# Kernel optimization log

Measured on AMD Instinct MI355X. Metric: run time of the kernel, lower is better.

The kernel has to match this reference:

```python
import jax, jax.numpy as jnp
import numpy as np

EPS = 1e-6
LOG2PI = float(np.log(2.0 * np.pi))


def gauss_lp(x, mu, lv):
    """Diagonal Gaussian log prob. x:[B,D], mu:[K,D], lv:[K,D] -> [B,K]."""
    inv_var = jnp.exp(-lv)                          # [K,D]
    d = x[:, None, :] - mu[None, :, :]              # [B,K,D]
    quad = jnp.sum(d * d * inv_var[None], axis=-1)  # [B,K]
    logdet = jnp.sum(lv, axis=-1)[None]             # [1,K]
    D = mu.shape[-1]
    return -0.5 * (quad + logdet + D * LOG2PI)


def setup_inputs() -> dict:
    key = jax.random.key(0)
    ks = jax.random.split(key, 9)
    T, B, S, A, OBS, CTL = 200, 256, 256, 16, 128, 16
    return {
        "x": jax.random.normal(ks[0], (T, B, OBS), jnp.float32),
        "u": jax.random.normal(ks[1], (T, B, CTL), jnp.float32),
        "obs_mu": jax.random.normal(ks[2], (S, OBS), jnp.float32),
        "obs_lv": 0.1 * jax.random.normal(ks[3], (S, OBS), jnp.float32),
        "ctl_mu": jax.random.normal(ks[4], (A, CTL), jnp.float32),
        "ctl_lv": 0.1 * jax.random.normal(ks[5], (A, CTL), jnp.float32),
        "trans_logits": jax.random.normal(ks[6], (A, S, S), jnp.float32),
        "pi0_logits": jax.random.normal(ks[7], (S,), jnp.float32),
        "act_prior": jax.random.normal(ks[8], (S, A), jnp.float32),
    }


def reference(x, u, obs_mu, obs_lv, ctl_mu, ctl_lv, trans_logits, pi0_logits, act_prior):
    """HMM forward algorithm (ContinuousGaussianHMM._forward).

    Returns:
      alpha_b: [T, B, S] state forward messages
      alpha_a: [T-1, B, A] action forward messages
    """
    S = obs_mu.shape[0]
    trans = jax.nn.softmax(trans_logits, axis=-1)      # [A,S,S]
    log_pi0 = jax.nn.log_softmax(pi0_logits)           # [S]

    # t = 0: initial state prior + observation likelihood
    b0 = jax.nn.softmax(gauss_lp(x[0], obs_mu, obs_lv) + log_pi0[None], axis=-1)  # [B,S]

    def step(b, xu):
        x_t, u_t = xu
        # action prior from belief: softmax(b @ act_prior)
        a_prior = jax.nn.softmax(b @ act_prior, axis=-1)                           # [B,A]
        # ctl_model.infer: posterior over actions given control u_t
        a_t = jax.nn.softmax(gauss_lp(u_t, ctl_mu, ctl_lv) + jnp.log(a_prior + EPS), axis=-1)  # [B,A]
        # action-conditioned transition applied to belief
        m = jnp.einsum('bi,kij->bkj', b, trans)                                    # [B,A,S]
        # original: sum_i(trans*b + eps) => einsum + S*eps
        logp_z = jnp.log(jnp.einsum('bk,bkj->bj', a_t, m) + S * EPS)               # [B,S]
        b_next = jax.nn.softmax(gauss_lp(x_t, obs_mu, obs_lv) + logp_z, axis=-1)   # [B,S]
        return b_next, (b_next, a_t)

    _, (bs, a_s) = jax.lax.scan(step, b0, (x[1:], u[:-1]))
    alpha_b = jnp.concatenate([b0[None], bs], axis=0)   # [T,B,S]
    alpha_a = a_s                                       # [T-1,B,A]
    return alpha_b, alpha_a
```

## Files before the change

kernel.cpp:

```cpp
#include <hip/hip_runtime.h>
#include <hip/hip_bf16.h>
#include <stdint.h>

#define T_STEPS 200
#define BATCH   256
#define NS      256
#define NA      16
#define DOBS    128
#define DCTL    16
#define LOG2PI  1.8378770664093453f
#define EPS_F   1e-6f
#define MINI(a,b) ((a)<(b)?(a):(b))

typedef float f32x4 __attribute__((ext_vector_type(4)));
typedef int   i32x4 __attribute__((ext_vector_type(4)));
typedef short s16x8 __attribute__((ext_vector_type(8)));
typedef short s16x4 __attribute__((ext_vector_type(4)));

static __device__ __forceinline__ unsigned short f2bf(float f) {
    union { float f; unsigned u; } v; v.f = f;
    unsigned u = v.u;
    u += 0x7fffu + ((u >> 16) & 1u);
    return (unsigned short)(u >> 16);
}

static __device__ __forceinline__ void ld4_mall(const float* base,
                                                f32x4& a, f32x4& b, f32x4& c, f32x4& d) {
    asm volatile(
        "global_load_dwordx4 %0, %4, off offset:0 sc0 sc1\n\t"
        "global_load_dwordx4 %1, %4, off offset:1024 sc0 sc1\n\t"
        "global_load_dwordx4 %2, %4, off offset:2048 sc0 sc1\n\t"
        "global_load_dwordx4 %3, %4, off offset:3072 sc0 sc1\n\t"
        "s_waitcnt vmcnt(0)"
        : "=&v"(a), "=&v"(b), "=&v"(c), "=&v"(d)
        : "v"(base)
        : "memory");
}
static __device__ __forceinline__ void st_mall(float* p, f32x4 v) {
    asm volatile("global_store_dwordx4 %0, %1, off sc0 sc1" :: "v"(p), "v"(v) : "memory");
}
static __device__ __forceinline__ void st_flag(int* p, int v) {
    asm volatile("global_store_dword %0, %1, off sc0 sc1" :: "v"(p), "v"(v) : "memory");
}
static __device__ __forceinline__ int min16(const int* fp) {
    i32x4 a, b, c, d;
    asm volatile(
        "global_load_dwordx4 %0, %4, off offset:0 sc0 sc1\n\t"
        "global_load_dwordx4 %1, %4, off offset:16 sc0 sc1\n\t"
        "global_load_dwordx4 %2, %4, off offset:32 sc0 sc1\n\t"
        "global_load_dwordx4 %3, %4, off offset:48 sc0 sc1\n\t"
        "s_waitcnt vmcnt(0)"
        : "=&v"(a), "=&v"(b), "=&v"(c), "=&v"(d)
        : "v"(fp)
        : "memory");
    int m = MINI(MINI(a[0], a[1]), MINI(a[2], a[3]));
    m = MINI(m, MINI(MINI(b[0], b[1]), MINI(b[2], b[3])));
    m = MINI(m, MINI(MINI(c[0], c[1]), MINI(c[2], c[3])));
    m = MINI(m, MINI(MINI(d[0], d[1]), MINI(d[2], d[3])));
    return m;
}

__global__ __launch_bounds__(128) void k_prep_obs(const float* __restrict__ obs_mu,
                                                  const float* __restrict__ obs_lv,
                                                  float* __restrict__ WT,
                                                  float* __restrict__ Cs) {
    int s = blockIdx.x, d = threadIdx.x;
    float lv = obs_lv[s * DOBS + d];
    float mu = obs_mu[s * DOBS + d];
    float iv = expf(-lv);
    WT[d * NS + s]          = -0.5f * iv;
    WT[(DOBS + d) * NS + s] = mu * iv;
    float part = mu * mu * iv + lv;
    for (int m = 1; m < 64; m <<= 1) part += __shfl_xor(part, m, 64);
    __shared__ float red[2];
    if ((threadIdx.x & 63) == 0) red[threadIdx.x >> 6] = part;
    __syncthreads();
    if (threadIdx.x == 0) Cs[s] = -0.5f * (red[0] + red[1] + DOBS * LOG2PI);
}

__global__ __launch_bounds__(256) void k_prep_ctl(const float* __restrict__ cmu,
                                                  const float* __restrict__ clv,
                                                  float* __restrict__ cw1,
                                                  float* __restrict__ cw2,
                                                  float* __restrict__ cc) {
    int t = threadIdx.x;
    int a = t >> 4, d = t & 15;
    float lv = clv[a * DCTL + d];
    float mu = cmu[a * DCTL + d];
    float iv = expf(-lv);
    cw1[t] = -0.5f * iv;
    cw2[t] = mu * iv;
    float part = mu * mu * iv + lv;
    for (int m = 1; m < 16; m <<= 1) part += __shfl_xor(part, m, 64);
    if (d == 0) cc[a] = -0.5f * (part + DCTL * LOG2PI);
}

__global__ __launch_bounds__(64) void k_prep_pi0(const float* __restrict__ pl,
                                                 float* __restrict__ lpi0) {
    int l = threadIdx.x;
    float v[4]; float m = -1e30f;
    for (int k = 0; k < 4; k++) { v[k] = pl[l + 64 * k]; m = fmaxf(m, v[k]); }
    for (int mm = 1; mm < 64; mm <<= 1) m = fmaxf(m, __shfl_xor(m, mm, 64));
    float ssum = 0.f;
    for (int k = 0; k < 4; k++) ssum += expf(v[k] - m);
    for (int mm = 1; mm < 64; mm <<= 1) ssum += __shfl_xor(ssum, mm, 64);
    float ls = logf(ssum);
    for (int k = 0; k < 4; k++) lpi0[l + 64 * k] = v[k] - m - ls;
}

__global__ __launch_bounds__(256) void k_zero(int* __restrict__ f) {
    st_flag(f + threadIdx.x, 0);
}

__global__ __launch_bounds__(256) void k_trans(const float* __restrict__ tl,
                                               __hip_bfloat16* __restrict__ TRf) {
    int wave = threadIdx.x >> 6, lane = threadIdx.x & 63;
    int row = blockIdx.x * 4 + wave;
    int a = row >> 8, i = row & 255;
    const float* src = tl + (size_t)row * NS;
    float v[4]; float m = -1e30f;
    for (int k = 0; k < 4; k++) { v[k] = src[lane + 64 * k]; m = fmaxf(m, v[k]); }
    for (int mm = 1; mm < 64; mm <<= 1) m = fmaxf(m, __shfl_xor(m, mm, 64));
    float ssum = 0.f; float ev[4];
    for (int k = 0; k < 4; k++) { ev[k] = expf(v[k] - m); ssum += ev[k]; }
    for (int mm = 1; mm < 64; mm <<= 1) ssum += __shfl_xor(ssum, mm, 64);
    float inv = 1.f / ssum;
    int kk = i >> 5;
    int lsub = ((i >> 3) & 3) * 16 + a;
    int e = i & 7;
    for (int k = 0; k < 4; k++) {
        int j = lane + 64 * k;
        float p = ev[k] * inv;
        TRf[((size_t)(j * 8 + kk) * 64 + lsub) * 8 + e] = __float2bfloat16(p);
    }
}

__global__ __launch_bounds__(64) void k_prep_ap(const float* __restrict__ ap,
                                                __hip_bfloat16* __restrict__ APh,
                                                __hip_bfloat16* __restrict__ APl) {
    int kk = blockIdx.x, lane = threadIdx.x;
    for (int e = 0; e < 8; e++) {
        int i = kk * 32 + (lane >> 4) * 8 + e;
        int a = lane & 15;
        float v = ap[i * NA + a];
        __hip_bfloat16 hb = __float2bfloat16(v);
        float hi = __bfloat162float(hb);
        APh[(kk * 64 + lane) * 8 + e] = hb;
        APl[(kk * 64 + lane) * 8 + e] = __float2bfloat16(v - hi);
    }
}

__global__ __launch_bounds__(256) void k_obslp(const float* __restrict__ x,
                                               const float* __restrict__ WT,
                                               const float* __restrict__ Cs,
                                               float* __restrict__ obs) {
    __shared__ float f[32 * 256];
    int r0 = blockIdx.x * 32;
    for (int idx = threadIdx.x; idx < 32 * DOBS; idx += 256) {
        int r = idx >> 7, d = idx & 127;
        float v = x[(size_t)(r0 + r) * DOBS + d];
        f[r * 256 + d] = v * v;
        f[r * 256 + 128 + d] = v;
    }
    __syncthreads();
    int s = threadIdx.x;
    float acc[32];
#pragma unroll
    for (int r = 0; r < 32; r++) acc[r] = 0.f;
    for (int d4 = 0; d4 < 64; d4++) {
        float w0 = WT[(d4 * 4 + 0) * NS + s];
        float w1 = WT[(d4 * 4 + 1) * NS + s];
        float w2 = WT[(d4 * 4 + 2) * NS + s];
        float w3 = WT[(d4 * 4 + 3) * NS + s];
#pragma unroll
        for (int r = 0; r < 32; r++) {
            f32x4 fv = *reinterpret_cast<const f32x4*>(&f[r * 256 + d4 * 4]);
            acc[r] += fv.x * w0 + fv.y * w1 + fv.z * w2 + fv.w * w3;
        }
    }
    float c = Cs[s];
#pragma unroll
    for (int r = 0; r < 32; r++) obs[(size_t)(r0 + r) * NS + s] = acc[r] + c;
}

__global__ __launch_bounds__(256) void k_ctllp(const float* __restrict__ u,
                                               const float* __restrict__ cw1,
                                               const float* __restrict__ cw2,
                                               const float* __restrict__ cc,
                                               float* __restrict__ ctl) {
    int idx = blockIdx.x * 256 + threadIdx.x;
    int r = idx >> 4, a = idx & 15;
    const float* ur = u + (size_t)r * DCTL;
    const float* w1 = cw1 + a * DCTL;
    const float* w2 = cw2 + a * DCTL;
    float acc = cc[a];
#pragma unroll
    for (int d = 0; d < 16; d++) {
        float uv = ur[d];
        acc += uv * uv * w1[d] + uv * w2[d];
    }
    ctl[idx] = acc;
}

struct ScanArgs {
    const float* obs;
    const float* ctlp;
    const float* lpi0;
    const __hip_bfloat16* TRf;
    const __hip_bfloat16* APh;
    const __hip_bfloat16* APl;
    float* lgA;
    float* lgB;
    float* out_ab;
    float* out_aa;
    int*   flags;
};

__global__ __launch_bounds__(256, 1) void k_scan_p(ScanArgs A) {
    const int bid  = blockIdx.x;
    const int bt   = bid >> 4;
    const int jt   = bid & 15;
    const int tid  = threadIdx.x;
    const int wv   = tid >> 6, lane = tid & 63;
    const int kgrp = lane >> 4, arow = lane & 15;
    const int b0   = bt * 16;
    const int* fp  = A.flags + bt * 16;

    __shared__ __align__(16) char PLb[16 * 512];
    __shared__ float out_t[16][16];

    s16x8 bfr[4][8];
#pragma unroll
    for (int q = 0; q < 4; q++) {
        int ct = jt * 16 + wv * 4 + q;
#pragma unroll
        for (int kk = 0; kk < 8; kk++)
            bfr[q][kk] = *((const s16x8*)A.TRf + (size_t)(ct * 8 + kk) * 64 + lane);
    }
    s16x8 aph[8], apl[8];
#pragma unroll
    for (int kk = 0; kk < 8; kk++) {
        aph[kk] = *((const s16x8*)A.APh + kk * 64 + lane);
        apl[kk] = *((const s16x8*)A.APl + kk * 64 + lane);
    }
    f32x4 lp0 = *(const f32x4*)&A.lpi0[lane * 4];

    const float* obs_pf_p = A.obs + ((size_t)BATCH + b0 + kgrp * 4) * NS + jt * 16 + wv * 4;
    const float* ctl_p    = A.ctlp + ((size_t)b0 + kgrp * 4) * NA + arow;
    float*       ab_p     = A.out_ab + ((size_t)b0 + wv * 4) * NS + lane * 4;
    float*       aa_p     = A.out_aa + ((size_t)b0 + kgrp * 4) * NA + arow;
    const float* lgA_ld   = A.lgA + ((size_t)b0 + wv * 4) * NS + lane * 4;
    const float* lgB_ld   = A.lgB + ((size_t)b0 + wv * 4) * NS + lane * 4;
    float*       lgA_st   = A.lgA + ((size_t)b0 + (lane >> 2)) * NS + jt * 16 + (lane & 3) * 4;
    float*       lgB_st   = A.lgB + ((size_t)b0 + (lane >> 2)) * NS + jt * 16 + (lane & 3) * 4;

    for (int s = 0; s < T_STEPS - 1; s++) {
        float obs_pf[16];
#pragma unroll
        for (int q2 = 0; q2 < 4; q2++)
#pragma unroll
            for (int r = 0; r < 4; r++)
                obs_pf[q2 * 4 + r] = obs_pf_p[r * NS + q2];
        float ctl_pf[4];
#pragma unroll
        for (int q = 0; q < 4; q++)
            ctl_pf[q] = ctl_p[q * NA];

        if (s > 0) {
            if (tid == 0) {
                while (min16(fp) < s) __builtin_amdgcn_s_sleep(1);
            }
            __syncthreads();
        }

        f32x4 V[4];
        if (s == 0) {
#pragma unroll
            for (int q = 0; q < 4; q++) {
                f32x4 o = *(const f32x4*)&A.obs[(size_t)(b0 + wv * 4 + q) * NS + lane * 4];
                V[q] = o + lp0;
            }
        } else {
            ld4_mall((s & 1) ? lgB_ld : lgA_ld, V[0], V[1], V[2], V[3]);
        }
#pragma unroll
        for (int q = 0; q < 4; q++) {
            int r = wv * 4 + q;
            float m = fmaxf(fmaxf(V[q].x, V[q].y), fmaxf(V[q].z, V[q].w));
            for (int mm = 1; mm < 64; mm <<= 1) m = fmaxf(m, __shfl_xor(m, mm, 64));
            float e0 = __expf(V[q].x - m), e1 = __expf(V[q].y - m);
            float e2 = __expf(V[q].z - m), e3 = __expf(V[q].w - m);
            float ss = (e0 + e1) + (e2 + e3);
            for (int mm = 1; mm < 64; mm <<= 1) ss += __shfl_xor(ss, mm, 64);
            float inv = 1.f / ss;
            float p0 = e0 * inv, p1 = e1 * inv, p2 = e2 * inv, p3 = e3 * inv;
            if ((lane >> 2) == jt) {
                f32x4 pv = {p0, p1, p2, p3};
                *(f32x4*)&ab_p[q * NS] = pv;
            }
            s16x4 sv;
            sv[0] = (short)f2bf(p0); sv[1] = (short)f2bf(p1);
            sv[2] = (short)f2bf(p2); sv[3] = (short)f2bf(p3);
            *(s16x4*)(PLb + r * 512 + ((lane * 8) ^ ((r & 7) << 4))) = sv;
        }
        __syncthreads();

        s16x8 afr[8];
        {
            int sw = (arow & 7) << 4;
#pragma unroll
            for (int kk = 0; kk < 8; kk++)
                afr[kk] = *(const s16x8*)(PLb + arow * 512 + ((kk * 64 + kgrp * 16) ^ sw));
        }

        f32x4 g = {0.f, 0.f, 0.f, 0.f};
#pragma unroll
        for (int kk = 0; kk < 8; kk++)
            g = __builtin_amdgcn_mfma_f32_16x16x32_bf16(afr[kk], aph[kk], g, 0, 0, 0);
#pragma unroll
        for (int kk = 0; kk < 8; kk++)
            g = __builtin_amdgcn_mfma_f32_16x16x32_bf16(afr[kk], apl[kk], g, 0, 0, 0);

        float at[4];
#pragma unroll
        for (int q = 0; q < 4; q++) {
            float gv = g[q];
            float m = gv;
            for (int mm = 1; mm < 16; mm <<= 1) m = fmaxf(m, __shfl_xor(m, mm, 64));
            float e1 = __expf(gv - m);
            float s1 = e1;
            for (int mm = 1; mm < 16; mm <<= 1) s1 += __shfl_xor(s1, mm, 64);
            float apr = e1 / s1;
            float al = ctl_pf[q] + __logf(apr + EPS_F);
            float m2 = al;
            for (int mm = 1; mm < 16; mm <<= 1) m2 = fmaxf(m2, __shfl_xor(m2, mm, 64));
            float e2 = __expf(al - m2);
            float s2 = e2;
            for (int mm = 1; mm < 16; mm <<= 1) s2 += __shfl_xor(s2, mm, 64);
            at[q] = e2 / s2;
            if (jt == 0)
                aa_p[q * NA] = at[q];
        }

#pragma unroll
        for (int q2 = 0; q2 < 4; q2++) {
            f32x4 acc = {0.f, 0.f, 0.f, 0.f};
#pragma unroll
            for (int kk = 0; kk < 8; kk++)
                acc = __builtin_amdgcn_mfma_f32_16x16x32_bf16(afr[kk], bfr[q2][kk], acc, 0, 0, 0);
#pragma unroll
            for (int r = 0; r < 4; r++) {
                float vv = acc[r] * at[r];
                for (int mm = 1; mm < 16; mm <<= 1) vv += __shfl_xor(vv, mm, 64);
                if (arow == 0)
                    out_t[kgrp * 4 + r][wv * 4 + q2] =
                        obs_pf[q2 * 4 + r] + __logf(vv + NS * EPS_F);
            }
        }
        __syncthreads();

        if (wv == 0) {
            f32x4 val = *(const f32x4*)&out_t[lane >> 2][(lane & 3) * 4];
            st_mall((s & 1) ? lgA_st : lgB_st, val);
            asm volatile("s_waitcnt vmcnt(0)" ::: "memory");
            if (lane == 0)
                st_flag((int*)&A.flags[bt * 16 + jt], s + 1);
        }
        obs_pf_p += (size_t)BATCH * NS;
        ctl_p    += (size_t)BATCH * NA;
        ab_p     += (size_t)BATCH * NS;
        aa_p     += (size_t)BATCH * NA;
    }

    if (tid == 0) {
        while (min16(fp) < T_STEPS - 1) __builtin_amdgcn_s_sleep(1);
    }
    __syncthreads();
    f32x4 V[4];
    ld4_mall(((T_STEPS - 1) & 1) ? lgB_ld : lgA_ld, V[0], V[1], V[2], V[3]);
#pragma unroll
    for (int q = 0; q < 4; q++) {
        float m = fmaxf(fmaxf(V[q].x, V[q].y), fmaxf(V[q].z, V[q].w));
        for (int mm = 1; mm < 64; mm <<= 1) m = fmaxf(m, __shfl_xor(m, mm, 64));
        float e0 = __expf(V[q].x - m), e1 = __expf(V[q].y - m);
        float e2 = __expf(V[q].z - m), e3 = __expf(V[q].w - m);
        float ss = (e0 + e1) + (e2 + e3);
        for (int mm = 1; mm < 64; mm <<= 1) ss += __shfl_xor(ss, mm, 64);
        float inv = 1.f / ss;
        if ((lane >> 2) == jt) {
            f32x4 pv = {e0 * inv, e1 * inv, e2 * inv, e3 * inv};
            *(f32x4*)&ab_p[q * NS] = pv;
        }
    }
}

extern "C" void kernel_launch(void* const* d_in, const int* in_sizes, int n_in,
                              void* d_out, int out_size, void* d_ws, size_t ws_size,
                              hipStream_t stream) {
    const float* x            = (const float*)d_in[0];
    const float* u            = (const float*)d_in[1];
    const float* obs_mu       = (const float*)d_in[2];
    const float* obs_lv       = (const float*)d_in[3];
    const float* ctl_mu       = (const float*)d_in[4];
    const float* ctl_lv       = (const float*)d_in[5];
    const float* trans_logits = (const float*)d_in[6];
    const float* pi0_logits   = (const float*)d_in[7];
    const float* act_prior    = (const float*)d_in[8];

    float* out_ab = (float*)d_out;
    float* out_aa = out_ab + (size_t)T_STEPS * BATCH * NS;

    char* w = (char*)d_ws;
    size_t off = 0;
    auto alloc = [&](size_t bytes) -> void* {
        void* pp = w + off;
        off += (bytes + 255) & ~(size_t)255;
        return pp;
    };
    float* WT   = (float*)alloc((size_t)256 * 256 * 4);
    float* Cs   = (float*)alloc(256 * 4);
    float* cw1  = (float*)alloc(256 * 4);
    float* cw2  = (float*)alloc(256 * 4);
    float* cc   = (float*)alloc(16 * 4);
    float* lpi0 = (float*)alloc(256 * 4);
    __hip_bfloat16* TRf = (__hip_bfloat16*)alloc((size_t)4096 * 256 * 2);
    __hip_bfloat16* APh = (__hip_bfloat16*)alloc((size_t)8 * 64 * 8 * 2);
    __hip_bfloat16* APl = (__hip_bfloat16*)alloc((size_t)8 * 64 * 8 * 2);
    float* obs  = (float*)alloc((size_t)T_STEPS * BATCH * NS * 4);
    float* ctlp = (float*)alloc((size_t)(T_STEPS - 1) * BATCH * NA * 4);
    float* lgA  = (float*)alloc((size_t)BATCH * NS * 4);
    float* lgB  = (float*)alloc((size_t)BATCH * NS * 4);
    int*   flags = (int*)alloc(256 * 4);
    if (off > ws_size) return;

    k_zero<<<1, 256, 0, stream>>>(flags);
    k_prep_obs<<<256, 128, 0, stream>>>(obs_mu, obs_lv, WT, Cs);
    k_prep_ctl<<<1, 256, 0, stream>>>(ctl_mu, ctl_lv, cw1, cw2, cc);
    k_prep_pi0<<<1, 64, 0, stream>>>(pi0_logits, lpi0);
    k_trans<<<1024, 256, 0, stream>>>(trans_logits, TRf);
    k_prep_ap<<<8, 64, 0, stream>>>(act_prior, APh, APl);
    k_obslp<<<1600, 256, 0, stream>>>(x, WT, Cs, obs);
    k_ctllp<<<3184, 256, 0, stream>>>(u, cw1, cw2, cc, ctlp);

    ScanArgs args;
    args.obs = obs; args.ctlp = ctlp; args.lpi0 = lpi0;
    args.TRf = TRf; args.APh = APh; args.APl = APl;
    args.lgA = lgA; args.lgB = lgB;
    args.out_ab = out_ab; args.out_aa = out_aa; args.flags = flags;
    k_scan_p<<<256, 256, 0, stream>>>(args);
}
```

Before: 2.366 ms.

## Split each scan block into two interleaved 8-row batch groups with blocked exchange layout

Each persistent scan block now handles two independent groups of 8 batch rows, 32 groups in total, and alternates their steps. While one group waits on its cross-block flags, the other can compute, which is meant to hide synchronisation latency between blocks. The lgA/lgB exchange buffers move to a per-tile blocked layout so each block stores one contiguous 512-byte chunk. MFMA tiles are half padded with zero rows, which wastes compute and adds extra barriers per step.

```diff
diff --git a/kernel.cpp b/kernel.cpp
--- a/kernel.cpp
+++ b/kernel.cpp
@@ -24,17 +24,12 @@
     return (unsigned short)(u >> 16);
 }
 
-static __device__ __forceinline__ void ld4_mall(const float* base,
-                                                f32x4& a, f32x4& b, f32x4& c, f32x4& d) {
+static __device__ __forceinline__ void ld2_mall(const float* base, f32x4& a, f32x4& b) {
     asm volatile(
-        "global_load_dwordx4 %0, %4, off offset:0 sc0 sc1\n\t"
-        "global_load_dwordx4 %1, %4, off offset:1024 sc0 sc1\n\t"
-        "global_load_dwordx4 %2, %4, off offset:2048 sc0 sc1\n\t"
-        "global_load_dwordx4 %3, %4, off offset:3072 sc0 sc1\n\t"
+        "global_load_dwordx4 %0, %2, off offset:0 sc0 sc1\n\t"
+        "global_load_dwordx4 %1, %2, off offset:64 sc0 sc1\n\t"
         "s_waitcnt vmcnt(0)"
-        : "=&v"(a), "=&v"(b), "=&v"(c), "=&v"(d)
-        : "v"(base)
-        : "memory");
+        : "=&v"(a), "=&v"(b) : "v"(base) : "memory");
 }
 static __device__ __forceinline__ void st_mall(float* p, f32x4 v) {
     asm volatile("global_store_dwordx4 %0, %1, off sc0 sc1" :: "v"(p), "v"(v) : "memory");
@@ -108,7 +103,7 @@
     for (int k = 0; k < 4; k++) lpi0[l + 64 * k] = v[k] - m - ls;
 }
 
-__global__ __launch_bounds__(256) void k_zero(int* __restrict__ f) {
+__global__ __launch_bounds__(512) void k_zero(int* __restrict__ f) {
     st_flag(f + threadIdx.x, 0);
 }
 
@@ -216,170 +211,133 @@
     int*   flags;
 };
 
-__global__ __launch_bounds__(256, 1) void k_scan_p(ScanArgs A) {
-    const int bid  = blockIdx.x;
-    const int bt   = bid >> 4;
-    const int jt   = bid & 15;
-    const int tid  = threadIdx.x;
-    const int wv   = tid >> 6, lane = tid & 63;
-    const int kgrp = lane >> 4, arow = lane & 15;
-    const int b0   = bt * 16;
-    const int* fp  = A.flags + bt * 16;
-
-    __shared__ __align__(16) char PLb[16 * 512];
-    __shared__ float out_t[16][16];
-
-    s16x8 bfr[4][8];
-#pragma unroll
-    for (int q = 0; q < 4; q++) {
-        int ct = jt * 16 + wv * 4 + q;
-#pragma unroll
-        for (int kk = 0; kk < 8; kk++)
-            bfr[q][kk] = *((const s16x8*)A.TRf + (size_t)(ct * 8 + kk) * 64 + lane);
-    }
-    s16x8 aph[8], apl[8];
-#pragma unroll
-    for (int kk = 0; kk < 8; kk++) {
-        aph[kk] = *((const s16x8*)A.APh + kk * 64 + lane);
-        apl[kk] = *((const s16x8*)A.APl + kk * 64 + lane);
-    }
-    f32x4 lp0 = *(const f32x4*)&A.lpi0[lane * 4];
-
-    const float* obs_pf_p = A.obs + ((size_t)BATCH + b0 + kgrp * 4) * NS + jt * 16 + wv * 4;
-    const float* ctl_p    = A.ctlp + ((size_t)b0 + kgrp * 4) * NA + arow;
-    float*       ab_p     = A.out_ab + ((size_t)b0 + wv * 4) * NS + lane * 4;
-    float*       aa_p     = A.out_aa + ((size_t)b0 + kgrp * 4) * NA + arow;
-    const float* lgA_ld   = A.lgA + ((size_t)b0 + wv * 4) * NS + lane * 4;
-    const float* lgB_ld   = A.lgB + ((size_t)b0 + wv * 4) * NS + lane * 4;
-    float*       lgA_st   = A.lgA + ((size_t)b0 + (lane >> 2)) * NS + jt * 16 + (lane & 3) * 4;
-    float*       lgB_st   = A.lgB + ((size_t)b0 + (lane >> 2)) * NS + jt * 16 + (lane & 3) * 4;
-
-    for (int s = 0; s < T_STEPS - 1; s++) {
-        float obs_pf[16];
-#pragma unroll
-        for (int q2 = 0; q2 < 4; q2++)
-#pragma unroll
-            for (int r = 0; r < 4; r++)
-                obs_pf[q2 * 4 + r] = obs_pf_p[r * NS + q2];
-        float ctl_pf[4];
-#pragma unroll
-        for (int q = 0; q < 4; q++)
-            ctl_pf[q] = ctl_p[q * NA];
-
-        if (s > 0) {
-            if (tid == 0) {
-                while (min16(fp) < s) __builtin_amdgcn_s_sleep(1);
-            }
-            __syncthreads();
-        }
-
-        f32x4 V[4];
-        if (s == 0) {
-#pragma unroll
-            for (int q = 0; q < 4; q++) {
-                f32x4 o = *(const f32x4*)&A.obs[(size_t)(b0 + wv * 4 + q) * NS + lane * 4];
-                V[q] = o + lp0;
-            }
-        } else {
-            ld4_mall((s & 1) ? lgB_ld : lgA_ld, V[0], V[1], V[2], V[3]);
-        }
-#pragma unroll
-        for (int q = 0; q < 4; q++) {
-            int r = wv * 4 + q;
-            float m = fmaxf(fmaxf(V[q].x, V[q].y), fmaxf(V[q].z, V[q].w));
-            for (int mm = 1; mm < 64; mm <<= 1) m = fmaxf(m, __shfl_xor(m, mm, 64));
-            float e0 = __expf(V[q].x - m), e1 = __expf(V[q].y - m);
-            float e2 = __expf(V[q].z - m), e3 = __expf(V[q].w - m);
-            float ss = (e0 + e1) + (e2 + e3);
-            for (int mm = 1; mm < 64; mm <<= 1) ss += __shfl_xor(ss, mm, 64);
-            float inv = 1.f / ss;
-            float p0 = e0 * inv, p1 = e1 * inv, p2 = e2 * inv, p3 = e3 * inv;
-            if ((lane >> 2) == jt) {
-                f32x4 pv = {p0, p1, p2, p3};
-                *(f32x4*)&ab_p[q * NS] = pv;
-            }
-            s16x4 sv;
-            sv[0] = (short)f2bf(p0); sv[1] = (short)f2bf(p1);
-            sv[2] = (short)f2bf(p2); sv[3] = (short)f2bf(p3);
-            *(s16x4*)(PLb + r * 512 + ((lane * 8) ^ ((r & 7) << 4))) = sv;
+static __device__ __forceinline__ void scan_step(
+    int s, int jt, int lane, int wv, int kgrp, int arow,
+    const s16x8 (&bfr)[4][8], const s16x8 (&aph)[8], const s16x8 (&apl)[8],
+    const f32x4& lp0,
+    const float*& obs_pf_p, const float*& ctl_p, float*& ab_p, float*& aa_p,
+    const float* obs0, const float* lgA_ld, const float* lgB_ld,
+    float* lgA_st, float* lgB_st,
+    const int* flagline, int* ownslot,
+    char* PLb, float (*out_t)[16])
+{
+    f32x4 obs_pfv[4];
+#pragma unroll
+    for (int r = 0; r < 4; r++)
+        obs_pfv[r] = *(const f32x4*)&obs_pf_p[r * NS];
+    float ctl_pf[4];
+#pragma unroll
+    for (int q = 0; q < 4; q++)
+        ctl_pf[q] = ctl_p[q * NA];
+
+    if (s > 0) {
+        if (threadIdx.x == 0) {
+            while (min16(flagline) < s) __builtin_amdgcn_s_sleep(1);
         }
         __syncthreads();
-
-        s16x8 afr[8];
-        {
-            int sw = (arow & 7) << 4;
-#pragma unroll
-            for (int kk = 0; kk < 8; kk++)
-                afr[kk] = *(const s16x8*)(PLb + arow * 512 + ((kk * 64 + kgrp * 16) ^ sw));
+    }
+
+    f32x4 V[2];
+    if (s == 0) {
+        V[0] = *(const f32x4*)&obs0[0]  + lp0;
+        V[1] = *(const f32x4*)&obs0[NS] + lp0;
+    } else {
+        ld2_mall((s & 1) ? lgB_ld : lgA_ld, V[0], V[1]);
+    }
+#pragma unroll
+    for (int q = 0; q < 2; q++) {
+        int r = wv * 2 + q;
+        float m = fmaxf(fmaxf(V[q].x, V[q].y), fmaxf(V[q].z, V[q].w));
+        for (int mm = 1; mm < 64; mm <<= 1) m = fmaxf(m, __shfl_xor(m, mm, 64));
+        float e0 = __expf(V[q].x - m), e1 = __expf(V[q].y - m);
+        float e2 = __expf(V[q].z - m), e3 = __expf(V[q].w - m);
+        float ss = (e0 + e1) + (e2 + e3);
+        for (int mm = 1; mm < 64; mm <<= 1) ss += __shfl_xor(ss, mm, 64);
+        float inv = 1.f / ss;
+        float p0 = e0 * inv, p1 = e1 * inv, p2 = e2 * inv, p3 = e3 * inv;
+        if ((lane >> 2) == jt) {
+            f32x4 pv = {p0, p1, p2, p3};
+            *(f32x4*)&ab_p[q * NS] = pv;
         }
-
-        f32x4 g = {0.f, 0.f, 0.f, 0.f};
+        s16x4 sv;
+        sv[0] = (short)f2bf(p0); sv[1] = (short)f2bf(p1);
+        sv[2] = (short)f2bf(p2); sv[3] = (short)f2bf(p3);
+        *(s16x4*)(PLb + r * 512 + ((lane * 8) ^ (r << 4))) = sv;
+    }
+    __syncthreads();
+
+    s16x8 afr[8];
+    {
+        int sw = (arow & 7) << 4;
 #pragma unroll
         for (int kk = 0; kk < 8; kk++)
-            g = __builtin_amdgcn_mfma_f32_16x16x32_bf16(afr[kk], aph[kk], g, 0, 0, 0);
+            afr[kk] = *(const s16x8*)(PLb + arow * 512 + ((kk * 64 + kgrp * 16) ^ sw));
+    }
+
+    f32x4 gh = {0.f, 0.f, 0.f, 0.f}, gl = {0.f, 0.f, 0.f, 0.f};
+#pragma unroll
+    for (int kk = 0; kk < 8; kk++) {
+        gh = __builtin_amdgcn_mfma_f32_16x16x32_bf16(afr[kk], aph[kk], gh, 0, 0, 0);
+        gl = __builtin_amdgcn_mfma_f32_16x16x32_bf16(afr[kk], apl[kk], gl, 0, 0, 0);
+    }
+    float at[4];
+#pragma unroll
+    for (int q = 0; q < 4; q++) {
+        float gv = gh[q] + gl[q];
+        float m = gv;
+        for (int mm = 1; mm < 16; mm <<= 1) m = fmaxf(m, __shfl_xor(m, mm, 64));
+        float e1 = __expf(gv - m);
+        float s1 = e1;
+        for (int mm = 1; mm < 16; mm <<= 1) s1 += __shfl_xor(s1, mm, 64);
+        float apr = e1 / s1;
+        float al = ctl_pf[q] + __logf(apr + EPS_F);
+        float m2 = al;
+        for (int mm = 1; mm < 16; mm <<= 1) m2 = fmaxf(m2, __shfl_xor(m2, mm, 64));
+        float e2 = __expf(al - m2);
+        float s2 = e2;
+        for (int mm = 1; mm < 16; mm <<= 1) s2 += __shfl_xor(s2, mm, 64);
+        at[q] = e2 / s2;
+        if (jt == 0 && kgrp < 2)
+            aa_p[q * NA] = at[q];
+    }
+
+#pragma unroll
+    for (int q2 = 0; q2 < 4; q2++) {
+        f32x4 acc = {0.f, 0.f, 0.f, 0.f};
 #pragma unroll
         for (int kk = 0; kk < 8; kk++)
-            g = __builtin_amdgcn_mfma_f32_16x16x32_bf16(afr[kk], apl[kk], g, 0, 0, 0);
-
-        float at[4];
-#pragma unroll
-        for (int q = 0; q < 4; q++) {
-            float gv = g[q];
-            float m = gv;
-            for (int mm = 1; mm < 16; mm <<= 1) m = fmaxf(m, __shfl_xor(m, mm, 64));
-            float e1 = __expf(gv - m);
-            float s1 = e1;
-            for (int mm = 1; mm < 16; mm <<= 1) s1 += __shfl_xor(s1, mm, 64);
-            float apr = e1 / s1;
-            float al = ctl_pf[q] + __logf(apr + EPS_F);
-            float m2 = al;
-            for (int mm = 1; mm < 16; mm <<= 1) m2 = fmaxf(m2, __shfl_xor(m2, mm, 64));
-            float e2 = __expf(al - m2);
-            float s2 = e2;
-            for (int mm = 1; mm < 16; mm <<= 1) s2 += __shfl_xor(s2, mm, 64);
-            at[q] = e2 / s2;
-            if (jt == 0)
-                aa_p[q * NA] = at[q];
+            acc = __builtin_amdgcn_mfma_f32_16x16x32_bf16(afr[kk], bfr[q2][kk], acc, 0, 0, 0);
+#pragma unroll
+        for (int r = 0; r < 4; r++) {
+            float vv = acc[r] * at[r];
+            for (int mm = 1; mm < 16; mm <<= 1) vv += __shfl_xor(vv, mm, 64);
+            if (arow == 0 && kgrp < 2)
+                out_t[kgrp * 4 + r][wv * 4 + q2] =
+                    obs_pfv[r][q2] + __logf(vv + NS * EPS_F);
         }
-
-#pragma unroll
-        for (int q2 = 0; q2 < 4; q2++) {
-            f32x4 acc = {0.f, 0.f, 0.f, 0.f};
-#pragma unroll
-            for (int kk = 0; kk < 8; kk++)
-                acc = __builtin_amdgcn_mfma_f32_16x16x32_bf16(afr[kk], bfr[q2][kk], acc, 0, 0, 0);
-#pragma unroll
-            for (int r = 0; r < 4; r++) {
-                float vv = acc[r] * at[r];
-                for (int mm = 1; mm < 16; mm <<= 1) vv += __shfl_xor(vv, mm, 64);
-                if (arow == 0)
-                    out_t[kgrp * 4 + r][wv * 4 + q2] =
-                        obs_pf[q2 * 4 + r] + __logf(vv + NS * EPS_F);
-            }
-        }
-        __syncthreads();
-
-        if (wv == 0) {
-            f32x4 val = *(const f32x4*)&out_t[lane >> 2][(lane & 3) * 4];
-            st_mall((s & 1) ? lgA_st : lgB_st, val);
-            asm volatile("s_waitcnt vmcnt(0)" ::: "memory");
-            if (lane == 0)
-                st_flag((int*)&A.flags[bt * 16 + jt], s + 1);
-        }
-        obs_pf_p += (size_t)BATCH * NS;
-        ctl_p    += (size_t)BATCH * NA;
-        ab_p     += (size_t)BATCH * NS;
-        aa_p     += (size_t)BATCH * NA;
-    }
-
-    if (tid == 0) {
-        while (min16(fp) < T_STEPS - 1) __builtin_amdgcn_s_sleep(1);
-    }
-    __syncthreads();
-    f32x4 V[4];
-    ld4_mall(((T_STEPS - 1) & 1) ? lgB_ld : lgA_ld, V[0], V[1], V[2], V[3]);
-#pragma unroll
-    for (int q = 0; q < 4; q++) {
+    }
+    __syncthreads();
+
+    if (wv == 0 && lane < 32) {
+        f32x4 val = *(const f32x4*)&out_t[lane >> 2][(lane & 3) * 4];
+        st_mall(((s & 1) ? lgA_st : lgB_st) + lane * 4, val);
+        asm volatile("s_waitcnt vmcnt(0)" ::: "memory");
+        if (lane == 0)
+            st_flag(ownslot, s + 1);
+    }
+    obs_pf_p += (size_t)BATCH * NS;
+    ctl_p    += (size_t)BATCH * NA;
+    ab_p     += (size_t)BATCH * NS;
+    aa_p     += (size_t)BATCH * NA;
+}
+
+static __device__ __forceinline__ void final_softmax(
+    int jt, int lane, int wv, const float* ld_base, float* ab_p)
+{
+    f32x4 V[2];
+    ld2_mall(ld_base, V[0], V[1]);
+#pragma unroll
+    for (int q = 0; q < 2; q++) {
         float m = fmaxf(fmaxf(V[q].x, V[q].y), fmaxf(V[q].z, V[q].w));
         for (int mm = 1; mm < 64; mm <<= 1) m = fmaxf(m, __shfl_xor(m, mm, 64));
         float e0 = __expf(V[q].x - m), e1 = __expf(V[q].y - m);
@@ -392,6 +350,82 @@
             *(f32x4*)&ab_p[q * NS] = pv;
         }
     }
+}
+
+__global__ __launch_bounds__(256, 1) void k_scan_p(ScanArgs A) {
+    const int bid  = blockIdx.x;
+    const int btA  = bid >> 4;
+    const int btB  = btA + 16;
+    const int jt   = bid & 15;
+    const int tid  = threadIdx.x;
+    const int wv   = tid >> 6, lane = tid & 63;
+    const int kgrp = lane >> 4, arow = lane & 15;
+    const int b0A  = btA * 8, b0B = btB * 8;
+
+    __shared__ __align__(16) char PLbA[16 * 512];
+    __shared__ __align__(16) char PLbB[16 * 512];
+    __shared__ float outA[8][16], outB[8][16];
+
+    for (int i = tid; i < 1024; i += 256) {
+        ((int*)(PLbA + 4096))[i] = 0;
+        ((int*)(PLbB + 4096))[i] = 0;
+    }
+
+    s16x8 bfr[4][8];
+#pragma unroll
+    for (int q = 0; q < 4; q++) {
+        int ct = jt * 16 + wv * 4 + q;
+#pragma unroll
+        for (int kk = 0; kk < 8; kk++)
+            bfr[q][kk] = *((const s16x8*)A.TRf + (size_t)(ct * 8 + kk) * 64 + lane);
+    }
+    s16x8 aph[8], apl[8];
+#pragma unroll
+    for (int kk = 0; kk < 8; kk++) {
+        aph[kk] = *((const s16x8*)A.APh + kk * 64 + lane);
+        apl[kk] = *((const s16x8*)A.APl + kk * 64 + lane);
+    }
+    f32x4 lp0 = *(const f32x4*)&A.lpi0[lane * 4];
+    __syncthreads();
+
+    const int rclamp = (kgrp & 1) * 4;
+    const float* obs_pfA = A.obs + ((size_t)BATCH + b0A + rclamp) * NS + jt * 16 + wv * 4;
+    const float* obs_pfB = A.obs + ((size_t)BATCH + b0B + rclamp) * NS + jt * 16 + wv * 4;
+    const float* ctlA    = A.ctlp + ((size_t)b0A + rclamp) * NA + arow;
+    const float* ctlB    = A.ctlp + ((size_t)b0B + rclamp) * NA + arow;
+    float* abA = A.out_ab + ((size_t)b0A + wv * 2) * NS + lane * 4;
+    float* abB = A.out_ab + ((size_t)b0B + wv * 2) * NS + lane * 4;
+    float* aaA = A.out_aa + ((size_t)b0A + rclamp) * NA + arow;
+    float* aaB = A.out_aa + ((size_t)b0B + rclamp) * NA + arow;
+    const float* obs0A = A.obs + (size_t)(b0A + wv * 2) * NS + lane * 4;
+    const float* obs0B = A.obs + (size_t)(b0B + wv * 2) * NS + lane * 4;
+    const size_t ldoff_A = (size_t)btA * 2048 + (lane >> 2) * 128 + (wv * 2) * 16 + (lane & 3) * 4;
+    const size_t ldoff_B = (size_t)btB * 2048 + (lane >> 2) * 128 + (wv * 2) * 16 + (lane & 3) * 4;
+    const size_t stoff_A = (size_t)(btA * 16 + jt) * 128;
+    const size_t stoff_B = (size_t)(btB * 16 + jt) * 128;
+    const float* lgA_ldA = A.lgA + ldoff_A; const float* lgB_ldA = A.lgB + ldoff_A;
+    const float* lgA_ldB = A.lgA + ldoff_B; const float* lgB_ldB = A.lgB + ldoff_B;
+    float* lgA_stA = A.lgA + stoff_A; float* lgB_stA = A.lgB + stoff_A;
+    float* lgA_stB = A.lgA + stoff_B; float* lgB_stB = A.lgB + stoff_B;
+    const int* fpA = A.flags + btA * 16; int* osA = A.flags + btA * 16 + jt;
+    const int* fpB = A.flags + btB * 16; int* osB = A.flags + btB * 16 + jt;
+
+    for (int s = 0; s < T_STEPS - 1; s++) {
+        scan_step(s, jt, lane, wv, kgrp, arow, bfr, aph, apl, lp0,
+                  obs_pfA, ctlA, abA, aaA, obs0A,
+                  lgA_ldA, lgB_ldA, lgA_stA, lgB_stA, fpA, osA, PLbA, outA);
+        scan_step(s, jt, lane, wv, kgrp, arow, bfr, aph, apl, lp0,
+                  obs_pfB, ctlB, abB, aaB, obs0B,
+                  lgA_ldB, lgB_ldB, lgA_stB, lgB_stB, fpB, osB, PLbB, outB);
+    }
+
+    if (tid == 0) {
+        while (min16(fpA) < T_STEPS - 1) __builtin_amdgcn_s_sleep(1);
+        while (min16(fpB) < T_STEPS - 1) __builtin_amdgcn_s_sleep(1);
+    }
+    __syncthreads();
+    final_softmax(jt, lane, wv, ((T_STEPS - 1) & 1) ? lgB_ldA : lgA_ldA, abA);
+    final_softmax(jt, lane, wv, ((T_STEPS - 1) & 1) ? lgB_ldB : lgA_ldB, abB);
 }
 
 extern "C" void kernel_launch(void* const* d_in, const int* in_sizes, int n_in,
@@ -428,12 +462,12 @@
     __hip_bfloat16* APl = (__hip_bfloat16*)alloc((size_t)8 * 64 * 8 * 2);
     float* obs  = (float*)alloc((size_t)T_STEPS * BATCH * NS * 4);
     float* ctlp = (float*)alloc((size_t)(T_STEPS - 1) * BATCH * NA * 4);
-    float* lgA  = (float*)alloc((size_t)BATCH * NS * 4);
-    float* lgB  = (float*)alloc((size_t)BATCH * NS * 4);
-    int*   flags = (int*)alloc(256 * 4);
+    float* lgA  = (float*)alloc((size_t)32 * 16 * 128 * 4);
+    float* lgB  = (float*)alloc((size_t)32 * 16 * 128 * 4);
+    int*   flags = (int*)alloc(512 * 4);
     if (off > ws_size) return;
 
-    k_zero<<<1, 256, 0, stream>>>(flags);
+    k_zero<<<1, 512, 0, stream>>>(flags);
     k_prep_obs<<<256, 128, 0, stream>>>(obs_mu, obs_lv, WT, Cs);
     k_prep_ctl<<<1, 256, 0, stream>>>(ctl_mu, ctl_lv, cw1, cw2, cc);
     k_prep_pi0<<<1, 64, 0, stream>>>(pi0_logits, lpi0);
```

Measured after the change: 3.533 ms. 1.49x slower.

## Replace flag-based cross-block sync with NaN-sentinel polling on a 4-slot ring buffer

Applied to the files above, without the earlier changes.

Removes the per-step flag counters, the store-wait-then-flag-write sequence and the block-wide barrier that gated every step. Consumers now spin directly on the data buffer until it no longer holds NaN. A 4-deep ring of log-message buffers is pre-filled with NaN, and each slot is reset to NaN two steps ahead so producers never overwrite a slot still being read. It also splits the action-prior MFMA chain into two independent accumulators and vectorises the observation prefetch. The cost is extra buffer memory and reliance on stores landing in order and the NaN check being reliable; each wave also polls independently.

```diff
diff --git a/kernel.cpp b/kernel.cpp
--- a/kernel.cpp
+++ b/kernel.cpp
@@ -10,10 +10,8 @@
 #define DCTL    16
 #define LOG2PI  1.8378770664093453f
 #define EPS_F   1e-6f
-#define MINI(a,b) ((a)<(b)?(a):(b))
 
 typedef float f32x4 __attribute__((ext_vector_type(4)));
-typedef int   i32x4 __attribute__((ext_vector_type(4)));
 typedef short s16x8 __attribute__((ext_vector_type(8)));
 typedef short s16x4 __attribute__((ext_vector_type(4)));
 
@@ -38,26 +36,6 @@
 }
 static __device__ __forceinline__ void st_mall(float* p, f32x4 v) {
     asm volatile("global_store_dwordx4 %0, %1, off sc0 sc1" :: "v"(p), "v"(v) : "memory");
-}
-static __device__ __forceinline__ void st_flag(int* p, int v) {
-    asm volatile("global_store_dword %0, %1, off sc0 sc1" :: "v"(p), "v"(v) : "memory");
-}
-static __device__ __forceinline__ int min16(const int* fp) {
-    i32x4 a, b, c, d;
-    asm volatile(
-        "global_load_dwordx4 %0, %4, off offset:0 sc0 sc1\n\t"
-        "global_load_dwordx4 %1, %4, off offset:16 sc0 sc1\n\t"
-        "global_load_dwordx4 %2, %4, off offset:32 sc0 sc1\n\t"
-        "global_load_dwordx4 %3, %4, off offset:48 sc0 sc1\n\t"
-        "s_waitcnt vmcnt(0)"
-        : "=&v"(a), "=&v"(b), "=&v"(c), "=&v"(d)
-        : "v"(fp)
-        : "memory");
-    int m = MINI(MINI(a[0], a[1]), MINI(a[2], a[3]));
-    m = MINI(m, MINI(MINI(b[0], b[1]), MINI(b[2], b[3])));
-    m = MINI(m, MINI(MINI(c[0], c[1]), MINI(c[2], c[3])));
-    m = MINI(m, MINI(MINI(d[0], d[1]), MINI(d[2], d[3])));
-    return m;
 }
 
 __global__ __launch_bounds__(128) void k_prep_obs(const float* __restrict__ obs_mu,
@@ -108,8 +86,11 @@
     for (int k = 0; k < 4; k++) lpi0[l + 64 * k] = v[k] - m - ls;
 }
 
-__global__ __launch_bounds__(256) void k_zero(int* __restrict__ f) {
-    st_flag(f + threadIdx.x, 0);
+__global__ __launch_bounds__(256) void k_init(float* __restrict__ lg) {
+    int idx = blockIdx.x * 256 + threadIdx.x;
+    float nv = __int_as_float(0x7FC00000);
+    f32x4 n4 = {nv, nv, nv, nv};
+    st_mall(lg + (size_t)idx * 4, n4);
 }
 
 __global__ __launch_bounds__(256) void k_trans(const float* __restrict__ tl,
@@ -209,11 +190,9 @@
     const __hip_bfloat16* TRf;
     const __hip_bfloat16* APh;
     const __hip_bfloat16* APl;
-    float* lgA;
-    float* lgB;
+    float* lg;
     float* out_ab;
     float* out_aa;
-    int*   flags;
 };
 
 __global__ __launch_bounds__(256, 1) void k_scan_p(ScanArgs A) {
@@ -224,10 +203,12 @@
     const int wv   = tid >> 6, lane = tid & 63;
     const int kgrp = lane >> 4, arow = lane & 15;
     const int b0   = bt * 16;
-    const int* fp  = A.flags + bt * 16;
 
     __shared__ __align__(16) char PLb[16 * 512];
     __shared__ float out_t[16][16];
+
+    const float nv = __int_as_float(0x7FC00000);
+    const f32x4 n4 = {nv, nv, nv, nv};
 
     s16x8 bfr[4][8];
 #pragma unroll
@@ -249,40 +230,42 @@
     const float* ctl_p    = A.ctlp + ((size_t)b0 + kgrp * 4) * NA + arow;
     float*       ab_p     = A.out_ab + ((size_t)b0 + wv * 4) * NS + lane * 4;
     float*       aa_p     = A.out_aa + ((size_t)b0 + kgrp * 4) * NA + arow;
-    const float* lgA_ld   = A.lgA + ((size_t)b0 + wv * 4) * NS + lane * 4;
-    const float* lgB_ld   = A.lgB + ((size_t)b0 + wv * 4) * NS + lane * 4;
-    float*       lgA_st   = A.lgA + ((size_t)b0 + (lane >> 2)) * NS + jt * 16 + (lane & 3) * 4;
-    float*       lgB_st   = A.lgB + ((size_t)b0 + (lane >> 2)) * NS + jt * 16 + (lane & 3) * 4;
+    const float* obs0_p   = A.obs + (size_t)(b0 + wv * 4) * NS + lane * 4;
+    const float* lg_ld    = A.lg + ((size_t)b0 + wv * 4) * NS + lane * 4;
+    float*       lg_st    = A.lg + ((size_t)b0 + (lane >> 2)) * NS + jt * 16 + (lane & 3) * 4;
 
     for (int s = 0; s < T_STEPS - 1; s++) {
-        float obs_pf[16];
-#pragma unroll
-        for (int q2 = 0; q2 < 4; q2++)
-#pragma unroll
-            for (int r = 0; r < 4; r++)
-                obs_pf[q2 * 4 + r] = obs_pf_p[r * NS + q2];
+        f32x4 obs_pfv[4];
+#pragma unroll
+        for (int r = 0; r < 4; r++)
+            obs_pfv[r] = *(const f32x4*)&obs_pf_p[r * NS];
         float ctl_pf[4];
 #pragma unroll
         for (int q = 0; q < 4; q++)
             ctl_pf[q] = ctl_p[q * NA];
 
-        if (s > 0) {
-            if (tid == 0) {
-                while (min16(fp) < s) __builtin_amdgcn_s_sleep(1);
-            }
-            __syncthreads();
-        }
-
         f32x4 V[4];
         if (s == 0) {
 #pragma unroll
             for (int q = 0; q < 4; q++) {
-                f32x4 o = *(const f32x4*)&A.obs[(size_t)(b0 + wv * 4 + q) * NS + lane * 4];
+                f32x4 o = *(const f32x4*)&obs0_p[q * NS];
                 V[q] = o + lp0;
             }
         } else {
-            ld4_mall((s & 1) ? lgB_ld : lgA_ld, V[0], V[1], V[2], V[3]);
-        }
+            const float* rb = lg_ld + ((size_t)(s & 3) << 16);
+            for (;;) {
+                ld4_mall(rb, V[0], V[1], V[2], V[3]);
+                float chk = ((V[0].x + V[0].y) + (V[0].z + V[0].w))
+                          + ((V[1].x + V[1].y) + (V[1].z + V[1].w))
+                          + ((V[2].x + V[2].y) + (V[2].z + V[2].w))
+                          + ((V[3].x + V[3].y) + (V[3].z + V[3].w));
+                if (chk == chk) break;
+            }
+        }
+
+        if (s >= 2 && wv == 0)
+            st_mall(lg_st + ((size_t)((s + 2) & 3) << 16), n4);
+
 #pragma unroll
         for (int q = 0; q < 4; q++) {
             int r = wv * 4 + q;
@@ -313,18 +296,16 @@
                 afr[kk] = *(const s16x8*)(PLb + arow * 512 + ((kk * 64 + kgrp * 16) ^ sw));
         }
 
-        f32x4 g = {0.f, 0.f, 0.f, 0.f};
-#pragma unroll
-        for (int kk = 0; kk < 8; kk++)
-            g = __builtin_amdgcn_mfma_f32_16x16x32_bf16(afr[kk], aph[kk], g, 0, 0, 0);
-#pragma unroll
-        for (int kk = 0; kk < 8; kk++)
-            g = __builtin_amdgcn_mfma_f32_16x16x32_bf16(afr[kk], apl[kk], g, 0, 0, 0);
-
+        f32x4 gh = {0.f, 0.f, 0.f, 0.f}, gl = {0.f, 0.f, 0.f, 0.f};
+#pragma unroll
+        for (int kk = 0; kk < 8; kk++) {
+            gh = __builtin_amdgcn_mfma_f32_16x16x32_bf16(afr[kk], aph[kk], gh, 0, 0, 0);
+            gl = __builtin_amdgcn_mfma_f32_16x16x32_bf16(afr[kk], apl[kk], gl, 0, 0, 0);
+        }
         float at[4];
 #pragma unroll
         for (int q = 0; q < 4; q++) {
-            float gv = g[q];
+            float gv = gh[q] + gl[q];
             float m = gv;
             for (int mm = 1; mm < 16; mm <<= 1) m = fmaxf(m, __shfl_xor(m, mm, 64));
             float e1 = __expf(gv - m);
@@ -354,17 +335,14 @@
                 for (int mm = 1; mm < 16; mm <<= 1) vv += __shfl_xor(vv, mm, 64);
                 if (arow == 0)
                     out_t[kgrp * 4 + r][wv * 4 + q2] =
-                        obs_pf[q2 * 4 + r] + __logf(vv + NS * EPS_F);
+                        obs_pfv[r][q2] + __logf(vv + NS * EPS_F);
             }
         }
         __syncthreads();
 
         if (wv == 0) {
             f32x4 val = *(const f32x4*)&out_t[lane >> 2][(lane & 3) * 4];
-            st_mall((s & 1) ? lgA_st : lgB_st, val);
-            asm volatile("s_waitcnt vmcnt(0)" ::: "memory");
-            if (lane == 0)
-                st_flag((int*)&A.flags[bt * 16 + jt], s + 1);
+            st_mall(lg_st + ((size_t)((s + 1) & 3) << 16), val);
         }
         obs_pf_p += (size_t)BATCH * NS;
         ctl_p    += (size_t)BATCH * NA;
@@ -372,12 +350,18 @@
         aa_p     += (size_t)BATCH * NA;
     }
 
-    if (tid == 0) {
-        while (min16(fp) < T_STEPS - 1) __builtin_amdgcn_s_sleep(1);
-    }
-    __syncthreads();
     f32x4 V[4];
-    ld4_mall(((T_STEPS - 1) & 1) ? lgB_ld : lgA_ld, V[0], V[1], V[2], V[3]);
+    {
+        const float* rb = lg_ld + ((size_t)((T_STEPS - 1) & 3) << 16);
+        for (;;) {
+            ld4_mall(rb, V[0], V[1], V[2], V[3]);
+            float chk = ((V[0].x + V[0].y) + (V[0].z + V[0].w))
+                      + ((V[1].x + V[1].y) + (V[1].z + V[1].w))
+                      + ((V[2].x + V[2].y) + (V[2].z + V[2].w))
+                      + ((V[3].x + V[3].y) + (V[3].z + V[3].w));
+            if (chk == chk) break;
+        }
+    }
 #pragma unroll
     for (int q = 0; q < 4; q++) {
         float m = fmaxf(fmaxf(V[q].x, V[q].y), fmaxf(V[q].z, V[q].w));
@@ -428,12 +412,10 @@
     __hip_bfloat16* APl = (__hip_bfloat16*)alloc((size_t)8 * 64 * 8 * 2);
     float* obs  = (float*)alloc((size_t)T_STEPS * BATCH * NS * 4);
     float* ctlp = (float*)alloc((size_t)(T_STEPS - 1) * BATCH * NA * 4);
-    float* lgA  = (float*)alloc((size_t)BATCH * NS * 4);
-    float* lgB  = (float*)alloc((size_t)BATCH * NS * 4);
-    int*   flags = (int*)alloc(256 * 4);
+    float* lg   = (float*)alloc((size_t)4 * BATCH * NS * 4);
     if (off > ws_size) return;
 
-    k_zero<<<1, 256, 0, stream>>>(flags);
+    k_init<<<256, 256, 0, stream>>>(lg);
     k_prep_obs<<<256, 128, 0, stream>>>(obs_mu, obs_lv, WT, Cs);
     k_prep_ctl<<<1, 256, 0, stream>>>(ctl_mu, ctl_lv, cw1, cw2, cc);
     k_prep_pi0<<<1, 64, 0, stream>>>(pi0_logits, lpi0);
@@ -445,7 +427,7 @@
     ScanArgs args;
     args.obs = obs; args.ctlp = ctlp; args.lpi0 = lpi0;
     args.TRf = TRf; args.APh = APh; args.APl = APl;
-    args.lgA = lgA; args.lgB = lgB;
-    args.out_ab = out_ab; args.out_aa = out_aa; args.flags = flags;
+    args.lg = lg;
+    args.out_ab = out_ab; args.out_aa = out_aa;
     k_scan_p<<<256, 256, 0, stream>>>(args);
 }
```

After: 2.087 ms. 11.8% less time.
